# Kernel tuning notes

Hardware: AMD Instinct MI355X
Metric: run time of the kernel (lower is better)

Reference implementation:

```python
import jax, jax.numpy as jnp
import numpy as np

V, D, A = 100000, 128, 64
L, N, K = 3, 20000, 16


def setup_inputs() -> dict:
    key = jax.random.key(0)
    k1, k2, k3, k4, k5, k6 = jax.random.split(key, 6)
    Leaf_emb = jax.random.normal(k1, (V, D), dtype=jnp.float32)
    nodes = jax.random.randint(k2, (L, N), 0, V, dtype=jnp.int32)
    neighbors = jax.random.randint(k3, (L, N, K), 0, V, dtype=jnp.int32)
    masks = jnp.zeros((L, N, K), dtype=jnp.float32)  # additive mask, 0 = valid
    weights = jax.random.normal(k4, (L, N, K), dtype=jnp.float32)
    W_att = jax.random.uniform(k5, (2 * D, A), dtype=jnp.float32)
    b_att = jnp.zeros((A,), dtype=jnp.float32)
    v_att = jax.random.uniform(k6, (A,), dtype=jnp.float32)
    return {"Leaf_emb": Leaf_emb, "nodes": nodes, "neighbors": neighbors,
            "masks": masks, "weights": weights,
            "W_att": W_att, "b_att": b_att, "v_att": v_att}


def reference(Leaf_emb, nodes, neighbors, masks, weights, W_att, b_att, v_att):
    # Sequential over L tree levels (fixed, small): each level gathers node and
    # neighbor embeddings, scores neighbors with a 2-layer attention MLP,
    # combines masked-softmax attention with softmax'd structural weights,
    # sums neighbor embeddings and scatters the result back into W_tmp.
    W_tmp = Leaf_emb
    n_levels = nodes.shape[0]
    for i in range(n_levels):
        node = nodes[i]                      # [N] (constant across K in original)
        neighbor = neighbors[i]              # [N, K]
        mask = masks[i]                      # [N, K] additive
        weight = weights[i]                  # [N, K]
        node_tmp = Leaf_emb[node][:, None, :]          # [N, 1, D] from ORIGINAL emb
        neighbor_tmp = W_tmp[neighbor]                 # [N, K, D] from running emb
        node_b = jnp.broadcast_to(node_tmp, neighbor_tmp.shape)
        att_in = jnp.concatenate([node_b, neighbor_tmp], axis=2)  # [N, K, 2D]
        mlp = jax.nn.leaky_relu(att_in @ W_att + b_att, 0.01)     # [N, K, A]
        pre = mlp @ v_att                                         # [N, K]
        att = jax.nn.softmax(pre + mask, axis=1) * jax.nn.softmax(weight, axis=1)
        temp_emb = jnp.einsum('nkd,nk->nd', neighbor_tmp, att)    # [N, D]
        W_tmp = W_tmp.at[node].set(temp_emb)
    return W_tmp
```

## Files before the change

### kernel.cpp

```cpp
#include <hip/hip_runtime.h>
#include <math.h>

#define V 100000
#define D 128
#define A 64
#define LVLS 3
#define NN 20000
#define KK 16
#define BK 32
#define TM 96
#define ASTRIDE 34
#define BSTW 132
#define BK2 16
#define AST2 18
#define BST2 68
#define PSTRIDE 128

__global__ __launch_bounds__(256, 2)
void projall_kernel(const float* __restrict__ Leaf, const float* __restrict__ Watt,
                    const float* __restrict__ batt, float* __restrict__ projAll,
                    float* __restrict__ outp) {
    __shared__ float As[TM * ASTRIDE];
    __shared__ float Bs[BK * BSTW];
    int t = threadIdx.x;
    int tx = t & 15, ty = t >> 4;
    int r0 = blockIdx.x * TM;

    const float* srcp[3];
    int rg[3];
#pragma unroll
    for (int jj = 0; jj < 3; ++jj) {
        int r = r0 + (t >> 3) + 32 * jj;
        rg[jj] = r;
        int rr = r < V ? r : V - 1;
        srcp[jj] = Leaf + (size_t)rr * D + ((t & 7) << 2);
    }
    int bc = (t & 31) << 2;
    int bk0 = t >> 5;
    const float* bbase = (bc < 64) ? (Watt + bc)
                                   : (Watt + (size_t)128 * A + (bc - 64));

    float4 bv = *(const float4*)(batt + 4 * tx);
    float accA[6][4], accB[6][4];
#pragma unroll
    for (int i = 0; i < 6; ++i) {
        accA[i][0] = bv.x; accA[i][1] = bv.y; accA[i][2] = bv.z; accA[i][3] = bv.w;
        accB[i][0] = 0.f;  accB[i][1] = 0.f;  accB[i][2] = 0.f;  accB[i][3] = 0.f;
    }

    for (int k0 = 0; k0 < D; k0 += BK) {
#pragma unroll
        for (int jj = 0; jj < 3; ++jj) {
            float4 v = *(const float4*)(srcp[jj] + k0);
            *(float4*)&As[((t >> 3) + 32 * jj) * ASTRIDE + ((t & 7) << 2)] = v;
            if (rg[jj] < V)
                *(float4*)(outp + (size_t)rg[jj] * D + k0 + ((t & 7) << 2)) = v;
        }
#pragma unroll
        for (int ss = 0; ss < 4; ++ss)
            *(float4*)&Bs[(bk0 + 8 * ss) * BSTW + bc] =
                *(const float4*)(bbase + (size_t)(k0 + bk0 + 8 * ss) * A);
        __syncthreads();
#pragma unroll
        for (int kc = 0; kc < BK; kc += 4) {
            float4 b0 = *(const float4*)&Bs[(kc + 0) * BSTW + 4 * tx];
            float4 b1 = *(const float4*)&Bs[(kc + 1) * BSTW + 4 * tx];
            float4 b2 = *(const float4*)&Bs[(kc + 2) * BSTW + 4 * tx];
            float4 b3 = *(const float4*)&Bs[(kc + 3) * BSTW + 4 * tx];
            float4 c0 = *(const float4*)&Bs[(kc + 0) * BSTW + 64 + 4 * tx];
            float4 c1 = *(const float4*)&Bs[(kc + 1) * BSTW + 64 + 4 * tx];
            float4 c2 = *(const float4*)&Bs[(kc + 2) * BSTW + 64 + 4 * tx];
            float4 c3 = *(const float4*)&Bs[(kc + 3) * BSTW + 64 + 4 * tx];
#pragma unroll
            for (int i = 0; i < 6; ++i) {
                float4 a = *(const float4*)&As[(6 * ty + i) * ASTRIDE + kc];
                accA[i][0] = fmaf(a.x, b0.x, accA[i][0]);
                accA[i][0] = fmaf(a.y, b1.x, accA[i][0]);
                accA[i][0] = fmaf(a.z, b2.x, accA[i][0]);
                accA[i][0] = fmaf(a.w, b3.x, accA[i][0]);
                accA[i][1] = fmaf(a.x, b0.y, accA[i][1]);
                accA[i][1] = fmaf(a.y, b1.y, accA[i][1]);
                accA[i][1] = fmaf(a.z, b2.y, accA[i][1]);
                accA[i][1] = fmaf(a.w, b3.y, accA[i][1]);
                accA[i][2] = fmaf(a.x, b0.z, accA[i][2]);
                accA[i][2] = fmaf(a.y, b1.z, accA[i][2]);
                accA[i][2] = fmaf(a.z, b2.z, accA[i][2]);
                accA[i][2] = fmaf(a.w, b3.z, accA[i][2]);
                accA[i][3] = fmaf(a.x, b0.w, accA[i][3]);
                accA[i][3] = fmaf(a.y, b1.w, accA[i][3]);
                accA[i][3] = fmaf(a.z, b2.w, accA[i][3]);
                accA[i][3] = fmaf(a.w, b3.w, accA[i][3]);
                accB[i][0] = fmaf(a.x, c0.x, accB[i][0]);
                accB[i][0] = fmaf(a.y, c1.x, accB[i][0]);
                accB[i][0] = fmaf(a.z, c2.x, accB[i][0]);
                accB[i][0] = fmaf(a.w, c3.x, accB[i][0]);
                accB[i][1] = fmaf(a.x, c0.y, accB[i][1]);
                accB[i][1] = fmaf(a.y, c1.y, accB[i][1]);
                accB[i][1] = fmaf(a.z, c2.y, accB[i][1]);
                accB[i][1] = fmaf(a.w, c3.y, accB[i][1]);
                accB[i][2] = fmaf(a.x, c0.z, accB[i][2]);
                accB[i][2] = fmaf(a.y, c1.z, accB[i][2]);
                accB[i][2] = fmaf(a.z, c2.z, accB[i][2]);
                accB[i][2] = fmaf(a.w, c3.z, accB[i][2]);
                accB[i][3] = fmaf(a.x, c0.w, accB[i][3]);
                accB[i][3] = fmaf(a.y, c1.w, accB[i][3]);
                accB[i][3] = fmaf(a.z, c2.w, accB[i][3]);
                accB[i][3] = fmaf(a.w, c3.w, accB[i][3]);
            }
        }
        __syncthreads();
    }

#pragma unroll
    for (int i = 0; i < 6; ++i) {
        int gr = r0 + 6 * ty + i;
        if (gr < V) {
            float4 oA = make_float4(accA[i][0], accA[i][1], accA[i][2], accA[i][3]);
            float4 oB = make_float4(accB[i][0], accB[i][1], accB[i][2], accB[i][3]);
            *(float4*)(projAll + (size_t)gr * PSTRIDE + 4 * tx) = oA;
            *(float4*)(projAll + (size_t)gr * PSTRIDE + 64 + 4 * tx) = oB;
        }
    }
}

__global__ __launch_bounds__(256, 4)
void commit_kernel(const float* __restrict__ tmp, const float* __restrict__ Wmat,
                   const int* __restrict__ nodes_l, const int* __restrict__ claim,
                   float* __restrict__ outp, float* __restrict__ projAll, int do_proj) {
    __shared__ float As[64 * AST2];
    __shared__ float Bs[BK2 * BST2];
    int t = threadIdx.x;
    int tx = t & 15, ty = t >> 4;
    int r0 = blockIdx.x * 64;

    int ar = t >> 2;
    int ak = (t & 3) << 2;
    int r = r0 + ar;
    int rr = r < NN ? r : NN - 1;
    const float* asrc = tmp + (size_t)rr * D + ak;
    int vrow = nodes_l[rr];
    int win = (r < NN) && (claim[vrow] == rr);

    int bk = t >> 4;
    int bc = (t & 15) << 2;

    float acc[4][4];
#pragma unroll
    for (int i = 0; i < 4; ++i) {
        acc[i][0] = 0.f; acc[i][1] = 0.f; acc[i][2] = 0.f; acc[i][3] = 0.f;
    }

    float4 pa = *(const float4*)(asrc);
    float4 pb = make_float4(0.f, 0.f, 0.f, 0.f);
    if (do_proj) pb = *(const float4*)(Wmat + (size_t)bk * A + bc);

    for (int k0 = 0; k0 < D; k0 += BK2) {
        if (k0) __syncthreads();
        *(float4*)&As[ar * AST2 + ak] = pa;
        if (do_proj) *(float4*)&Bs[bk * BST2 + bc] = pb;
        if (win)
            *(float4*)(outp + (size_t)vrow * D + k0 + ak) = pa;
        __syncthreads();
        int kn = k0 + BK2;
        if (kn < D) {
            pa = *(const float4*)(asrc + kn);
            if (do_proj) pb = *(const float4*)(Wmat + (size_t)(kn + bk) * A + bc);
        }
        if (do_proj) {
#pragma unroll
            for (int kc = 0; kc < BK2; kc += 4) {
                float4 b0 = *(const float4*)&Bs[(kc + 0) * BST2 + 4 * tx];
                float4 b1 = *(const float4*)&Bs[(kc + 1) * BST2 + 4 * tx];
                float4 b2 = *(const float4*)&Bs[(kc + 2) * BST2 + 4 * tx];
                float4 b3 = *(const float4*)&Bs[(kc + 3) * BST2 + 4 * tx];
#pragma unroll
                for (int i = 0; i < 4; ++i) {
                    float4 a = *(const float4*)&As[(4 * ty + i) * AST2 + kc];
                    acc[i][0] = fmaf(a.x, b0.x, acc[i][0]);
                    acc[i][0] = fmaf(a.y, b1.x, acc[i][0]);
                    acc[i][0] = fmaf(a.z, b2.x, acc[i][0]);
                    acc[i][0] = fmaf(a.w, b3.x, acc[i][0]);
                    acc[i][1] = fmaf(a.x, b0.y, acc[i][1]);
                    acc[i][1] = fmaf(a.y, b1.y, acc[i][1]);
                    acc[i][1] = fmaf(a.z, b2.y, acc[i][1]);
                    acc[i][1] = fmaf(a.w, b3.y, acc[i][1]);
                    acc[i][2] = fmaf(a.x, b0.z, acc[i][2]);
                    acc[i][2] = fmaf(a.y, b1.z, acc[i][2]);
                    acc[i][2] = fmaf(a.z, b2.z, acc[i][2]);
                    acc[i][2] = fmaf(a.w, b3.z, acc[i][2]);
                    acc[i][3] = fmaf(a.x, b0.w, acc[i][3]);
                    acc[i][3] = fmaf(a.y, b1.w, acc[i][3]);
                    acc[i][3] = fmaf(a.z, b2.w, acc[i][3]);
                    acc[i][3] = fmaf(a.w, b3.w, acc[i][3]);
                }
            }
        }
    }

    if (do_proj) {
#pragma unroll
        for (int i = 0; i < 4; ++i) {
            int gr = r0 + 4 * ty + i;
            if (gr < NN) {
                int v = nodes_l[gr];
                if (claim[v] == gr) {
                    float4 o = make_float4(acc[i][0], acc[i][1], acc[i][2], acc[i][3]);
                    *(float4*)(projAll + (size_t)v * PSTRIDE + 64 + 4 * tx) = o;
                }
            }
        }
    }
}

__global__ __launch_bounds__(256)
void attn_kernel(const float* __restrict__ Wc, const float* __restrict__ projAll,
                 const int* __restrict__ nodes_l, const int* __restrict__ neigh,
                 const float* __restrict__ maskp, const float* __restrict__ weightp,
                 const float* __restrict__ v_att, float* __restrict__ tmp) {
    int lane = threadIdx.x & 63;
    int n = blockIdx.x * 4 + (threadIdx.x >> 6);
    int k16 = lane & 15, q = lane >> 4;

    int   vnode = nodes_l[n];
    int   nbk = neigh[n * KK + k16];
    float wv  = weightp[n * KK + k16];
    float mk  = maskp[n * KK + k16];

    const float* npr = projAll + (size_t)vnode * PSTRIDE + q * 16;
    const float* var = v_att + q * 16;
    const float* pr  = projAll + (size_t)nbk * PSTRIDE + 64 + q * 16;

    float part = 0.f;
#pragma unroll
    for (int j = 0; j < 16; j += 4) {
        float4 npv = *(const float4*)(npr + j);
        float4 vav = *(const float4*)(var + j);
        float4 pv  = *(const float4*)(pr + j);
        float x;
        x = npv.x + pv.x; x = fmaxf(x, 0.01f * x); part = fmaf(x, vav.x, part);
        x = npv.y + pv.y; x = fmaxf(x, 0.01f * x); part = fmaf(x, vav.y, part);
        x = npv.z + pv.z; x = fmaxf(x, 0.01f * x); part = fmaf(x, vav.z, part);
        x = npv.w + pv.w; x = fmaxf(x, 0.01f * x); part = fmaf(x, vav.w, part);
    }
    part += __shfl_xor(part, 16);
    part += __shfl_xor(part, 32);
    float pre = part + mk;

    int half = lane >> 5, li = lane & 31;
    float4 e[8];
#pragma unroll
    for (int m = 0; m < 8; ++m) {
        int nb = __shfl(nbk, 2 * m + half);
        e[m] = *(const float4*)&Wc[(size_t)nb * D + 4 * li];
    }

    float mp = pre, mw = wv;
#pragma unroll
    for (int off = 8; off >= 1; off >>= 1) {
        mp = fmaxf(mp, __shfl_xor(mp, off));
        mw = fmaxf(mw, __shfl_xor(mw, off));
    }
    float ep = __expf(pre - mp), ew = __expf(wv - mw);
    float sp = ep, sw = ew;
#pragma unroll
    for (int off = 8; off >= 1; off >>= 1) {
        sp += __shfl_xor(sp, off);
        sw += __shfl_xor(sw, off);
    }
    float att = (ep / sp) * (ew / sw);

    float ax = 0.f, ay = 0.f, az = 0.f, aw = 0.f;
#pragma unroll
    for (int m = 0; m < 8; ++m) {
        float ak = __shfl(att, 2 * m + half);
        ax = fmaf(e[m].x, ak, ax); ay = fmaf(e[m].y, ak, ay);
        az = fmaf(e[m].z, ak, az); aw = fmaf(e[m].w, ak, aw);
    }
    ax += __shfl_xor(ax, 32); ay += __shfl_xor(ay, 32);
    az += __shfl_xor(az, 32); aw += __shfl_xor(aw, 32);
    if (half == 0) {
        float4 o = make_float4(ax, ay, az, aw);
        *(float4*)&tmp[(size_t)n * D + 4 * li] = o;
    }
}

__global__ void amax3_kernel(const int* __restrict__ nodes, int* __restrict__ claims, int total) {
    int i = blockIdx.x * 256 + threadIdx.x;
    if (i < total) {
        int lvl = i / NN, pos = i - lvl * NN;
        atomicMax(&claims[(size_t)lvl * V + nodes[i]], pos);
    }
}

extern "C" void kernel_launch(void* const* d_in, const int* in_sizes, int n_in,
                              void* d_out, int out_size, void* d_ws, size_t ws_size,
                              hipStream_t stream) {
    const float* Leaf    = (const float*)d_in[0];
    const int*   nodes   = (const int*)d_in[1];
    const int*   neigh   = (const int*)d_in[2];
    const float* masks   = (const float*)d_in[3];
    const float* weights = (const float*)d_in[4];
    const float* Watt    = (const float*)d_in[5];
    const float* batt    = (const float*)d_in[6];
    const float* vatt    = (const float*)d_in[7];
    float* out = (float*)d_out;

    char* ws = (char*)d_ws;
    float* projAll = (float*)ws;
    float* tmp     = (float*)(ws + (size_t)V * PSTRIDE * 4);
    int*   claims  = (int*)(ws + (size_t)(V * PSTRIDE + NN * D) * 4);

    hipMemsetAsync(claims, 0xFF, (size_t)LVLS * V * sizeof(int), stream);
    amax3_kernel<<<(LVLS * NN + 255) / 256, 256, 0, stream>>>(nodes, claims, LVLS * NN);
    projall_kernel<<<(V + TM - 1) / TM, 256, 0, stream>>>(Leaf, Watt, batt, projAll, out);

    for (int l = 0; l < LVLS; ++l) {
        const int* nodes_l = nodes + l * NN;
        attn_kernel<<<NN / 4, 256, 0, stream>>>(out, projAll, nodes_l,
                                                neigh + (size_t)l * NN * KK,
                                                masks + (size_t)l * NN * KK,
                                                weights + (size_t)l * NN * KK, vatt, tmp);
        commit_kernel<<<(NN + 63) / 64, 256, 0, stream>>>(
            tmp, Watt + (size_t)D * A, nodes_l, claims + (size_t)l * V, out, projAll,
            (l + 1 < LVLS) ? 1 : 0);
    }
}
```

Measured before the change: 301.0 us.

## Map two nodes per wavefront in attention kernel, one per half-wave

Restructures attn_kernel so each 64-lane wavefront handles two nodes (32 lanes each) instead of one, halving the grid size. Each half-wave computes the score with 2 lanes per neighbor over 32 attention dims. It then loops over all 16 neighbors serially to accumulate the weighted embedding, removing the cross-half reduction and the predicated half-wave store. The aim is to get full lane utilization on the gather/accumulate phase, at the cost of a longer dependent loop with loads interleaved rather than all issued up front.

```diff
diff --git a/kernel.cpp b/kernel.cpp
--- a/kernel.cpp
+++ b/kernel.cpp
@@ -217,22 +217,24 @@
                  const int* __restrict__ nodes_l, const int* __restrict__ neigh,
                  const float* __restrict__ maskp, const float* __restrict__ weightp,
                  const float* __restrict__ v_att, float* __restrict__ tmp) {
-    int lane = threadIdx.x & 63;
-    int n = blockIdx.x * 4 + (threadIdx.x >> 6);
-    int k16 = lane & 15, q = lane >> 4;
+    int t = threadIdx.x;
+    int lane = t & 63;
+    int n = blockIdx.x * 8 + ((t >> 6) << 1) + (lane >> 5);
+    int k16 = lane & 15;
+    int h = (lane >> 4) & 1;
 
     int   vnode = nodes_l[n];
     int   nbk = neigh[n * KK + k16];
     float wv  = weightp[n * KK + k16];
     float mk  = maskp[n * KK + k16];
 
-    const float* npr = projAll + (size_t)vnode * PSTRIDE + q * 16;
-    const float* var = v_att + q * 16;
-    const float* pr  = projAll + (size_t)nbk * PSTRIDE + 64 + q * 16;
+    const float* npr = projAll + (size_t)vnode * PSTRIDE + h * 32;
+    const float* var = v_att + h * 32;
+    const float* pr  = projAll + (size_t)nbk * PSTRIDE + 64 + h * 32;
 
     float part = 0.f;
 #pragma unroll
-    for (int j = 0; j < 16; j += 4) {
+    for (int j = 0; j < 32; j += 4) {
         float4 npv = *(const float4*)(npr + j);
         float4 vav = *(const float4*)(var + j);
         float4 pv  = *(const float4*)(pr + j);
@@ -243,16 +245,7 @@
         x = npv.w + pv.w; x = fmaxf(x, 0.01f * x); part = fmaf(x, vav.w, part);
     }
     part += __shfl_xor(part, 16);
-    part += __shfl_xor(part, 32);
     float pre = part + mk;
-
-    int half = lane >> 5, li = lane & 31;
-    float4 e[8];
-#pragma unroll
-    for (int m = 0; m < 8; ++m) {
-        int nb = __shfl(nbk, 2 * m + half);
-        e[m] = *(const float4*)&Wc[(size_t)nb * D + 4 * li];
-    }
 
     float mp = pre, mw = wv;
 #pragma unroll
@@ -269,19 +262,20 @@
     }
     float att = (ep / sp) * (ew / sw);
 
+    int li = lane & 31;
+    int nsel = lane & 32;
     float ax = 0.f, ay = 0.f, az = 0.f, aw = 0.f;
 #pragma unroll
-    for (int m = 0; m < 8; ++m) {
-        float ak = __shfl(att, 2 * m + half);
-        ax = fmaf(e[m].x, ak, ax); ay = fmaf(e[m].y, ak, ay);
-        az = fmaf(e[m].z, ak, az); aw = fmaf(e[m].w, ak, aw);
-    }
-    ax += __shfl_xor(ax, 32); ay += __shfl_xor(ay, 32);
-    az += __shfl_xor(az, 32); aw += __shfl_xor(aw, 32);
-    if (half == 0) {
-        float4 o = make_float4(ax, ay, az, aw);
-        *(float4*)&tmp[(size_t)n * D + 4 * li] = o;
-    }
+    for (int m = 0; m < KK; ++m) {
+        int src = nsel + m;
+        int nb   = __shfl(nbk, src);
+        float ak = __shfl(att, src);
+        float4 e = *(const float4*)&Wc[(size_t)nb * D + 4 * li];
+        ax = fmaf(e.x, ak, ax); ay = fmaf(e.y, ak, ay);
+        az = fmaf(e.z, ak, az); aw = fmaf(e.w, ak, aw);
+    }
+    float4 o = make_float4(ax, ay, az, aw);
+    *(float4*)&tmp[(size_t)n * D + 4 * li] = o;
 }
 
 __global__ void amax3_kernel(const int* __restrict__ nodes, int* __restrict__ claims, int total) {
@@ -316,7 +310,7 @@
 
     for (int l = 0; l < LVLS; ++l) {
         const int* nodes_l = nodes + l * NN;
-        attn_kernel<<<NN / 4, 256, 0, stream>>>(out, projAll, nodes_l,
+        attn_kernel<<<NN / 8, 256, 0, stream>>>(out, projAll, nodes_l,
                                                 neigh + (size_t)l * NN * KK,
                                                 masks + (size_t)l * NN * KK,
                                                 weights + (size_t)l * NN * KK, vatt, tmp);
```

Result: slower. 315.3 us (+4.7%).

## Replace tiled commit GEMM with per-node wavefront shuffle projection

Applied to the files above, without the earlier changes.

Replaces the shared-memory tiled GEMM commit kernel with a kernel that assigns one 64-lane wavefront per node. Non-winning nodes exit early. Each winning wavefront copies its row into the output and computes the 64-wide projection using lane shuffles and W reads served from cache. This drops the LDS staging and barriers and skips rows that lose the claim, at the cost of lower arithmetic reuse of W per load.

```diff
diff --git a/kernel.cpp b/kernel.cpp
--- a/kernel.cpp
+++ b/kernel.cpp
@@ -11,9 +11,6 @@
 #define TM 96
 #define ASTRIDE 34
 #define BSTW 132
-#define BK2 16
-#define AST2 18
-#define BST2 68
 #define PSTRIDE 128
 
 __global__ __launch_bounds__(256, 2)
@@ -123,93 +120,37 @@
     }
 }
 
-__global__ __launch_bounds__(256, 4)
-void commit_kernel(const float* __restrict__ tmp, const float* __restrict__ Wmat,
-                   const int* __restrict__ nodes_l, const int* __restrict__ claim,
-                   float* __restrict__ outp, float* __restrict__ projAll, int do_proj) {
-    __shared__ float As[64 * AST2];
-    __shared__ float Bs[BK2 * BST2];
-    int t = threadIdx.x;
-    int tx = t & 15, ty = t >> 4;
-    int r0 = blockIdx.x * 64;
-
-    int ar = t >> 2;
-    int ak = (t & 3) << 2;
-    int r = r0 + ar;
-    int rr = r < NN ? r : NN - 1;
-    const float* asrc = tmp + (size_t)rr * D + ak;
-    int vrow = nodes_l[rr];
-    int win = (r < NN) && (claim[vrow] == rr);
-
-    int bk = t >> 4;
-    int bc = (t & 15) << 2;
-
-    float acc[4][4];
-#pragma unroll
-    for (int i = 0; i < 4; ++i) {
-        acc[i][0] = 0.f; acc[i][1] = 0.f; acc[i][2] = 0.f; acc[i][3] = 0.f;
-    }
-
-    float4 pa = *(const float4*)(asrc);
-    float4 pb = make_float4(0.f, 0.f, 0.f, 0.f);
-    if (do_proj) pb = *(const float4*)(Wmat + (size_t)bk * A + bc);
-
-    for (int k0 = 0; k0 < D; k0 += BK2) {
-        if (k0) __syncthreads();
-        *(float4*)&As[ar * AST2 + ak] = pa;
-        if (do_proj) *(float4*)&Bs[bk * BST2 + bc] = pb;
-        if (win)
-            *(float4*)(outp + (size_t)vrow * D + k0 + ak) = pa;
-        __syncthreads();
-        int kn = k0 + BK2;
-        if (kn < D) {
-            pa = *(const float4*)(asrc + kn);
-            if (do_proj) pb = *(const float4*)(Wmat + (size_t)(kn + bk) * A + bc);
-        }
-        if (do_proj) {
-#pragma unroll
-            for (int kc = 0; kc < BK2; kc += 4) {
-                float4 b0 = *(const float4*)&Bs[(kc + 0) * BST2 + 4 * tx];
-                float4 b1 = *(const float4*)&Bs[(kc + 1) * BST2 + 4 * tx];
-                float4 b2 = *(const float4*)&Bs[(kc + 2) * BST2 + 4 * tx];
-                float4 b3 = *(const float4*)&Bs[(kc + 3) * BST2 + 4 * tx];
-#pragma unroll
-                for (int i = 0; i < 4; ++i) {
-                    float4 a = *(const float4*)&As[(4 * ty + i) * AST2 + kc];
-                    acc[i][0] = fmaf(a.x, b0.x, acc[i][0]);
-                    acc[i][0] = fmaf(a.y, b1.x, acc[i][0]);
-                    acc[i][0] = fmaf(a.z, b2.x, acc[i][0]);
-                    acc[i][0] = fmaf(a.w, b3.x, acc[i][0]);
-                    acc[i][1] = fmaf(a.x, b0.y, acc[i][1]);
-                    acc[i][1] = fmaf(a.y, b1.y, acc[i][1]);
-                    acc[i][1] = fmaf(a.z, b2.y, acc[i][1]);
-                    acc[i][1] = fmaf(a.w, b3.y, acc[i][1]);
-                    acc[i][2] = fmaf(a.x, b0.z, acc[i][2]);
-                    acc[i][2] = fmaf(a.y, b1.z, acc[i][2]);
-                    acc[i][2] = fmaf(a.z, b2.z, acc[i][2]);
-                    acc[i][2] = fmaf(a.w, b3.z, acc[i][2]);
-                    acc[i][3] = fmaf(a.x, b0.w, acc[i][3]);
-                    acc[i][3] = fmaf(a.y, b1.w, acc[i][3]);
-                    acc[i][3] = fmaf(a.z, b2.w, acc[i][3]);
-                    acc[i][3] = fmaf(a.w, b3.w, acc[i][3]);
-                }
-            }
-        }
-    }
-
-    if (do_proj) {
-#pragma unroll
-        for (int i = 0; i < 4; ++i) {
-            int gr = r0 + 4 * ty + i;
-            if (gr < NN) {
-                int v = nodes_l[gr];
-                if (claim[v] == gr) {
-                    float4 o = make_float4(acc[i][0], acc[i][1], acc[i][2], acc[i][3]);
-                    *(float4*)(projAll + (size_t)v * PSTRIDE + 64 + 4 * tx) = o;
-                }
-            }
-        }
-    }
+__global__ __launch_bounds__(256)
+void commit2_kernel(const float* __restrict__ tmp, const float* __restrict__ w2,
+                    const int* __restrict__ nodes_l, const int* __restrict__ claim,
+                    float* __restrict__ outp, float* __restrict__ projAll, int do_proj) {
+    int lane = threadIdx.x & 63;
+    int n = blockIdx.x * 4 + (threadIdx.x >> 6);
+    int li = lane & 31;
+
+    int v = nodes_l[n];
+    if (claim[v] != n) return;
+
+    float4 e = *(const float4*)&tmp[(size_t)n * D + 4 * li];
+    if (lane < 32)
+        *(float4*)&outp[(size_t)v * D + 4 * li] = e;
+
+    if (!do_proj) return;
+
+    const float* w2c = w2 + lane;
+    float p0 = 0.f, p1 = 0.f, p2 = 0.f, p3 = 0.f;
+#pragma unroll 8
+    for (int s = 0; s < 32; ++s) {
+        float bx = __shfl(e.x, s);
+        float by = __shfl(e.y, s);
+        float bz = __shfl(e.z, s);
+        float bw = __shfl(e.w, s);
+        p0 = fmaf(bx, w2c[(size_t)(4 * s + 0) * A], p0);
+        p1 = fmaf(by, w2c[(size_t)(4 * s + 1) * A], p1);
+        p2 = fmaf(bz, w2c[(size_t)(4 * s + 2) * A], p2);
+        p3 = fmaf(bw, w2c[(size_t)(4 * s + 3) * A], p3);
+    }
+    projAll[(size_t)v * PSTRIDE + 64 + lane] = (p0 + p1) + (p2 + p3);
 }
 
 __global__ __launch_bounds__(256)
@@ -320,7 +261,7 @@
                                                 neigh + (size_t)l * NN * KK,
                                                 masks + (size_t)l * NN * KK,
                                                 weights + (size_t)l * NN * KK, vatt, tmp);
-        commit_kernel<<<(NN + 63) / 64, 256, 0, stream>>>(
+        commit2_kernel<<<NN / 4, 256, 0, stream>>>(
             tmp, Watt + (size_t)D * A, nodes_l, claims + (size_t)l * V, out, projAll,
             (l + 1 < LVLS) ? 1 : 0);
     }
```

Measured after the change: 334.0 us. 1.11x slower.
